# Kernel tuning notes

Hardware: AMD Instinct MI355X
Metric: run time of the kernel (lower is better)

Reference implementation:

```python
import jax, jax.numpy as jnp
import numpy as np

B, H, LQ, LKV, D = 2, 4, 512, 512, 64


def setup_inputs() -> dict:
    key = jax.random.key(0)
    ks = jax.random.split(key, 6)
    queries = jax.random.normal(ks[0], (B, H, LQ, D), dtype=jnp.float32)
    keys = jax.random.normal(ks[1], (B, H, LKV, D), dtype=jnp.float32)
    values = jax.random.normal(ks[2], (B, H, LKV, D), dtype=jnp.float32)
    mask = jax.random.randint(ks[3], (B, LQ, LKV), 0, 2) > 0  # bool [B, Lq, Lkv]
    # linear_concat: weight [D, 2D] (normal std=0.02), bias zeros
    W_concat = jax.random.normal(ks[4], (D, 2 * D), dtype=jnp.float32) * 0.02
    b_concat = jnp.zeros((D,), dtype=jnp.float32)
    # linear_logit: weight [1, D] -> vector [D], bias scalar zero
    w_logit = jax.random.normal(ks[5], (D,), dtype=jnp.float32) * 0.02
    b_logit = jnp.zeros((), dtype=jnp.float32)
    return dict(queries=queries, keys=keys, values=values, mask=mask,
                W_concat=W_concat, b_concat=b_concat,
                w_logit=w_logit, b_logit=b_logit)


def reference(queries, keys, values, mask, W_concat, b_concat, w_logit, b_logit):
    d = queries.shape[-1]
    # cat(q, k) @ W.T == q @ W[:, :d].T + k @ W[:, d:].T  (exact split of the concat-linear)
    qp = jnp.einsum('bhqd,ed->bhqe', queries, W_concat[:, :d])   # [B,H,Lq,D]
    kp = jnp.einsum('bhkd,ed->bhke', keys, W_concat[:, d:])      # [B,H,Lkv,D]
    combined = jnp.tanh(qp[:, :, :, None, :] + kp[:, :, None, :, :] + b_concat)  # [B,H,Lq,Lkv,D]
    logits = jnp.einsum('bhqke,e->bhqk', combined, w_logit) + b_logit            # [B,H,Lq,Lkv]
    # mask handling: invert; rows fully masked get un-masked (avoid all -inf softmax)
    inv = ~mask  # [B,Lq,Lkv]
    inv = jnp.where(jnp.all(inv, axis=-1, keepdims=True), False, inv)
    inv = inv[:, None, :, :]  # broadcast over heads
    logits = jnp.where(inv, -jnp.inf, logits)
    weights = jax.nn.softmax(logits, axis=-1)
    if weights.shape[1] == 1:  # torch .squeeze(dim=1) semantics
        weights = jnp.squeeze(weights, axis=1)
    return weights
```

## Files before the change

kernel.cpp:

```cpp
#include <hip/hip_runtime.h>
#include <hip/hip_bf16.h>


#define NQROWS 4096

typedef float f32x2 __attribute__((ext_vector_type(2)));

__device__ __forceinline__ f32x2 fma2(f32x2 a, f32x2 b, f32x2 c) {
  return __builtin_elementwise_fma(a, b, c);
}
__device__ __forceinline__ f32x2 s2(float x) { return (f32x2){x, x}; }

__global__ __launch_bounds__(256) void proj_kernel(
    const float* __restrict__ Q, const float* __restrict__ K,
    const float* __restrict__ W, const float* __restrict__ bC,
    float* __restrict__ eq, float* __restrict__ ekt)
{
  const int t  = threadIdx.x;
  const int tr = t >> 6;
  const int e  = t & 63;
  const int rbase = blockIdx.x * 8;
  const bool isK = rbase >= NQROWS;
  const int r0 = isK ? rbase - NQROWS : rbase;
  const float* __restrict__ src = isK ? K : Q;
  const int off = isK ? 64 : 0;

  __shared__ float  srow[8][64];
  __shared__ float4 wsh[64][16];
  __shared__ float  trsp[64][9];

  for (int i = t; i < 8 * 64; i += 256)
    srow[i >> 6][i & 63] = src[(r0 + (i >> 6)) * 64 + (i & 63)];
  for (int i = t; i < 64 * 16; i += 256) {
    const int er = i >> 4, d4 = i & 15;
    wsh[er][d4 ^ (er & 7)] =
        reinterpret_cast<const float4*>(W + er * 128 + off)[d4];
  }
  __syncthreads();

  float acc0 = 0.f, acc1 = 0.f;
  const int rA = tr * 2;
  #pragma unroll
  for (int d4 = 0; d4 < 16; ++d4) {
    const float4 w4 = wsh[e][d4 ^ (e & 7)];
    const float4 s0 = *reinterpret_cast<const float4*>(&srow[rA + 0][d4 * 4]);
    const float4 s1 = *reinterpret_cast<const float4*>(&srow[rA + 1][d4 * 4]);
    acc0 = fmaf(s0.x, w4.x, acc0); acc0 = fmaf(s0.y, w4.y, acc0);
    acc0 = fmaf(s0.z, w4.z, acc0); acc0 = fmaf(s0.w, w4.w, acc0);
    acc1 = fmaf(s1.x, w4.x, acc1); acc1 = fmaf(s1.y, w4.y, acc1);
    acc1 = fmaf(s1.z, w4.z, acc1); acc1 = fmaf(s1.w, w4.w, acc1);
  }

  const float C2 = 2.8853900817779268f;
  if (!isK) {
    const float bias = bC[e];
    eq[(r0 + rA + 0) * 64 + e] = __builtin_amdgcn_exp2f((acc0 + bias) * C2);
    eq[(r0 + rA + 1) * 64 + e] = __builtin_amdgcn_exp2f((acc1 + bias) * C2);
  } else {
    trsp[e][rA + 0] = __builtin_amdgcn_exp2f(acc0 * C2);
    trsp[e][rA + 1] = __builtin_amdgcn_exp2f(acc1 * C2);
    __syncthreads();
    const int bh = r0 >> 9;
    const int k0 = r0 & 511;
    float* __restrict__ dst = ekt + bh * 64 * 512 + k0;
    #pragma unroll
    for (int iter = 0; iter < 2; ++iter) {
      const int i  = t + iter * 256;
      const int e2 = i >> 3, kk = i & 7;
      dst[e2 * 512 + kk] = trsp[e2][kk];
    }
  }
}

__global__ __launch_bounds__(256) void attn_kernel(
    const float* __restrict__ eq, const float* __restrict__ ekt,
    const float* __restrict__ wl, const int* __restrict__ mask,
    float* __restrict__ out)
{
  const int t  = threadIdx.x;
  const int c  = t;
  const int wv = t >> 6;
  const int ln = t & 63;
  const int bh = blockIdx.x & 7;
  const int qg = blockIdx.x >> 3;
  const int b  = bh >> 2;
  const int q0 = qg * 4;

  __shared__ float qsh[4][64];
  __shared__ float w2s[64];
  __shared__ float s_sm[4][4], s_sr[4][4];
  __shared__ int   s_any[4][4];

  if (t < 64) w2s[t] = -2.0f * wl[t];
  qsh[t >> 6][t & 63] = eq[(bh * 512 + q0 + (t >> 6)) * 64 + (t & 63)];
  __syncthreads();

  const f32x2* __restrict__ kq =
      reinterpret_cast<const f32x2*>(ekt + bh * 64 * 512) + c;

  f32x2 a0 = {0.f, 0.f}, a1 = {0.f, 0.f}, a2 = {0.f, 0.f}, a3 = {0.f, 0.f};
  const f32x2 one = {1.f, 1.f};

#define QK2(AC, QV)                                                           \
  {                                                                           \
    const f32x2 t0 = fma2(s2(QV.x), Ka, one);                                 \
    const f32x2 t1 = fma2(s2(QV.y), Kb, one);                                 \
    const f32x2 t2 = fma2(s2(QV.z), Kc, one);                                 \
    const f32x2 t3 = fma2(s2(QV.w), Kd, one);                                 \
    const f32x2 t01 = t0 * t1, t23 = t2 * t3;                                 \
    const f32x2 den = t01 * t23;                                              \
    const f32x2 n01 = fma2(s2(w4.x), t1, s2(w4.y) * t0);                      \
    const f32x2 n23 = fma2(s2(w4.z), t3, s2(w4.w) * t2);                      \
    const f32x2 num = fma2(n01, t23, n23 * t01);                              \
    f32x2 r;                                                                  \
    r.x = __builtin_amdgcn_rcpf(den.x);                                       \
    r.y = __builtin_amdgcn_rcpf(den.y);                                       \
    AC = fma2(num, r, AC);                                                    \
  }

  #pragma unroll 4
  for (int eb = 0; eb < 16; ++eb) {
    const f32x2 Ka = kq[(eb * 4 + 0) * 256];
    const f32x2 Kb = kq[(eb * 4 + 1) * 256];
    const f32x2 Kc = kq[(eb * 4 + 2) * 256];
    const f32x2 Kd = kq[(eb * 4 + 3) * 256];
    const float4 qa = *reinterpret_cast<const float4*>(&qsh[0][eb * 4]);
    const float4 qb = *reinterpret_cast<const float4*>(&qsh[1][eb * 4]);
    const float4 qc = *reinterpret_cast<const float4*>(&qsh[2][eb * 4]);
    const float4 qd = *reinterpret_cast<const float4*>(&qsh[3][eb * 4]);
    const float4 w4 = *reinterpret_cast<const float4*>(&w2s[eb * 4]);
    QK2(a0, qa)
    QK2(a1, qb)
    QK2(a2, qc)
    QK2(a3, qd)
  }

  const int* __restrict__ mb = mask + (b * 512 + q0) * 512 + 2 * c;
  const int2 mv0 = *reinterpret_cast<const int2*>(mb);
  const int2 mv1 = *reinterpret_cast<const int2*>(mb + 512);
  const int2 mv2 = *reinterpret_cast<const int2*>(mb + 1024);
  const int2 mv3 = *reinterpret_cast<const int2*>(mb + 1536);

  const float L2E = 1.4426950408889634f;
  f32x2 p0, p1, p2, p3;
  p0.x = __builtin_amdgcn_exp2f(a0.x * L2E);
  p0.y = __builtin_amdgcn_exp2f(a0.y * L2E);
  p1.x = __builtin_amdgcn_exp2f(a1.x * L2E);
  p1.y = __builtin_amdgcn_exp2f(a1.y * L2E);
  p2.x = __builtin_amdgcn_exp2f(a2.x * L2E);
  p2.y = __builtin_amdgcn_exp2f(a2.y * L2E);
  p3.x = __builtin_amdgcn_exp2f(a3.x * L2E);
  p3.y = __builtin_amdgcn_exp2f(a3.y * L2E);

  float sm0 = (mv0.x ? p0.x : 0.f) + (mv0.y ? p0.y : 0.f);
  float sm1 = (mv1.x ? p1.x : 0.f) + (mv1.y ? p1.y : 0.f);
  float sm2 = (mv2.x ? p2.x : 0.f) + (mv2.y ? p2.y : 0.f);
  float sm3 = (mv3.x ? p3.x : 0.f) + (mv3.y ? p3.y : 0.f);
  float sr0 = p0.x + p0.y;
  float sr1 = p1.x + p1.y;
  float sr2 = p2.x + p2.y;
  float sr3 = p3.x + p3.y;
  const int any0 = __any((mv0.x | mv0.y) != 0) ? 1 : 0;
  const int any1 = __any((mv1.x | mv1.y) != 0) ? 1 : 0;
  const int any2 = __any((mv2.x | mv2.y) != 0) ? 1 : 0;
  const int any3 = __any((mv3.x | mv3.y) != 0) ? 1 : 0;

  #pragma unroll
  for (int s = 1; s < 64; s <<= 1) {
    sm0 += __shfl_xor(sm0, s); sm1 += __shfl_xor(sm1, s);
    sm2 += __shfl_xor(sm2, s); sm3 += __shfl_xor(sm3, s);
    sr0 += __shfl_xor(sr0, s); sr1 += __shfl_xor(sr1, s);
    sr2 += __shfl_xor(sr2, s); sr3 += __shfl_xor(sr3, s);
  }
  if (ln == 0) {
    s_sm[wv][0] = sm0; s_sm[wv][1] = sm1; s_sm[wv][2] = sm2; s_sm[wv][3] = sm3;
    s_sr[wv][0] = sr0; s_sr[wv][1] = sr1; s_sr[wv][2] = sr2; s_sr[wv][3] = sr3;
    s_any[wv][0] = any0; s_any[wv][1] = any1;
    s_any[wv][2] = any2; s_any[wv][3] = any3;
  }
  __syncthreads();

#define ROWOUT(P, MV, I)                                                      \
  {                                                                           \
    const bool ra =                                                           \
        (s_any[0][I] | s_any[1][I] | s_any[2][I] | s_any[3][I]) != 0;         \
    const float sm =                                                          \
        (s_sm[0][I] + s_sm[1][I]) + (s_sm[2][I] + s_sm[3][I]);                \
    const float sr =                                                          \
        (s_sr[0][I] + s_sr[1][I]) + (s_sr[2][I] + s_sr[3][I]);                \
    const float inv = 1.0f / (ra ? sm : sr);                                  \
    float2 o2;                                                                \
    o2.x = ((!ra || MV.x) ? P.x : 0.f) * inv;                                 \
    o2.y = ((!ra || MV.y) ? P.y : 0.f) * inv;                                 \
    *reinterpret_cast<float2*>(                                               \
        out + (bh * 512 + q0 + (I)) * 512 + 2 * c) = o2;                      \
  }
  ROWOUT(p0, mv0, 0)
  ROWOUT(p1, mv1, 1)
  ROWOUT(p2, mv2, 2)
  ROWOUT(p3, mv3, 3)
}

extern "C" void kernel_launch(void* const* d_in, const int* in_sizes, int n_in,
                              void* d_out, int out_size, void* d_ws, size_t ws_size,
                              hipStream_t stream) {
  const float* Q  = (const float*)d_in[0];
  const float* K  = (const float*)d_in[1];
  const int*   M  = (const int*)d_in[3];
  const float* W  = (const float*)d_in[4];
  const float* bC = (const float*)d_in[5];
  const float* wl = (const float*)d_in[6];
  float* out = (float*)d_out;
  float* eqbuf  = (float*)d_ws;
  float* ektbuf = eqbuf + NQROWS * 64;

  proj_kernel<<<1024, 256, 0, stream>>>(Q, K, W, bC, eqbuf, ektbuf);
  attn_kernel<<<1024, 256, 0, stream>>>(eqbuf, ektbuf, wl, M, out);
}
```

Baseline: 27.38 us.

## Halve query rows per attention block, read q and w directly, fold scale into exp

The attention kernel now handles 2 query rows per block instead of 4 and launches twice as many blocks. The shared-memory staging of q rows and the scaled logit weights is removed along with its barrier; q and w are read straight from global memory with wave-uniform float4 loads. The -2 factor on w is folded into the exp2 constant instead. This raises parallelism and removes a sync, but each block now reuses each K load for only 2 query rows instead of 4, so total K traffic doubles.

```diff
diff --git a/kernel.cpp b/kernel.cpp
--- a/kernel.cpp
+++ b/kernel.cpp
@@ -82,23 +82,20 @@
   const int wv = t >> 6;
   const int ln = t & 63;
   const int bh = blockIdx.x & 7;
-  const int qg = blockIdx.x >> 3;
+  const int qp = blockIdx.x >> 3;
   const int b  = bh >> 2;
-  const int q0 = qg * 4;
+  const int q0 = qp * 2;
 
-  __shared__ float qsh[4][64];
-  __shared__ float w2s[64];
-  __shared__ float s_sm[4][4], s_sr[4][4];
-  __shared__ int   s_any[4][4];
+  __shared__ float s_sm[4][2], s_sr[4][2];
+  __shared__ int   s_any[4][2];
 
-  if (t < 64) w2s[t] = -2.0f * wl[t];
-  qsh[t >> 6][t & 63] = eq[(bh * 512 + q0 + (t >> 6)) * 64 + (t & 63)];
-  __syncthreads();
+  const float* __restrict__ eqA = eq + (bh * 512 + q0) * 64;
+  const float* __restrict__ eqB = eqA + 64;
 
   const f32x2* __restrict__ kq =
       reinterpret_cast<const f32x2*>(ekt + bh * 64 * 512) + c;
 
-  f32x2 a0 = {0.f, 0.f}, a1 = {0.f, 0.f}, a2 = {0.f, 0.f}, a3 = {0.f, 0.f};
+  f32x2 a0 = {0.f, 0.f}, a1 = {0.f, 0.f};
   const f32x2 one = {1.f, 1.f};
 
 #define QK2(AC, QV)                                                           \
@@ -124,59 +121,40 @@
     const f32x2 Kb = kq[(eb * 4 + 1) * 256];
     const f32x2 Kc = kq[(eb * 4 + 2) * 256];
     const f32x2 Kd = kq[(eb * 4 + 3) * 256];
-    const float4 qa = *reinterpret_cast<const float4*>(&qsh[0][eb * 4]);
-    const float4 qb = *reinterpret_cast<const float4*>(&qsh[1][eb * 4]);
-    const float4 qc = *reinterpret_cast<const float4*>(&qsh[2][eb * 4]);
-    const float4 qd = *reinterpret_cast<const float4*>(&qsh[3][eb * 4]);
-    const float4 w4 = *reinterpret_cast<const float4*>(&w2s[eb * 4]);
+    const float4 qa = *reinterpret_cast<const float4*>(eqA + eb * 4);
+    const float4 qb = *reinterpret_cast<const float4*>(eqB + eb * 4);
+    const float4 w4 = *reinterpret_cast<const float4*>(wl + eb * 4);
     QK2(a0, qa)
     QK2(a1, qb)
-    QK2(a2, qc)
-    QK2(a3, qd)
   }
 
   const int* __restrict__ mb = mask + (b * 512 + q0) * 512 + 2 * c;
   const int2 mv0 = *reinterpret_cast<const int2*>(mb);
   const int2 mv1 = *reinterpret_cast<const int2*>(mb + 512);
-  const int2 mv2 = *reinterpret_cast<const int2*>(mb + 1024);
-  const int2 mv3 = *reinterpret_cast<const int2*>(mb + 1536);
 
-  const float L2E = 1.4426950408889634f;
-  f32x2 p0, p1, p2, p3;
-  p0.x = __builtin_amdgcn_exp2f(a0.x * L2E);
-  p0.y = __builtin_amdgcn_exp2f(a0.y * L2E);
-  p1.x = __builtin_amdgcn_exp2f(a1.x * L2E);
-  p1.y = __builtin_amdgcn_exp2f(a1.y * L2E);
-  p2.x = __builtin_amdgcn_exp2f(a2.x * L2E);
-  p2.y = __builtin_amdgcn_exp2f(a2.y * L2E);
-  p3.x = __builtin_amdgcn_exp2f(a3.x * L2E);
-  p3.y = __builtin_amdgcn_exp2f(a3.y * L2E);
+  const float CM2 = -2.8853900817779268f;
+  f32x2 p0, p1;
+  p0.x = __builtin_amdgcn_exp2f(a0.x * CM2);
+  p0.y = __builtin_amdgcn_exp2f(a0.y * CM2);
+  p1.x = __builtin_amdgcn_exp2f(a1.x * CM2);
+  p1.y = __builtin_amdgcn_exp2f(a1.y * CM2);
 
   float sm0 = (mv0.x ? p0.x : 0.f) + (mv0.y ? p0.y : 0.f);
   float sm1 = (mv1.x ? p1.x : 0.f) + (mv1.y ? p1.y : 0.f);
-  float sm2 = (mv2.x ? p2.x : 0.f) + (mv2.y ? p2.y : 0.f);
-  float sm3 = (mv3.x ? p3.x : 0.f) + (mv3.y ? p3.y : 0.f);
   float sr0 = p0.x + p0.y;
   float sr1 = p1.x + p1.y;
-  float sr2 = p2.x + p2.y;
-  float sr3 = p3.x + p3.y;
   const int any0 = __any((mv0.x | mv0.y) != 0) ? 1 : 0;
   const int any1 = __any((mv1.x | mv1.y) != 0) ? 1 : 0;
-  const int any2 = __any((mv2.x | mv2.y) != 0) ? 1 : 0;
-  const int any3 = __any((mv3.x | mv3.y) != 0) ? 1 : 0;
 
   #pragma unroll
   for (int s = 1; s < 64; s <<= 1) {
     sm0 += __shfl_xor(sm0, s); sm1 += __shfl_xor(sm1, s);
-    sm2 += __shfl_xor(sm2, s); sm3 += __shfl_xor(sm3, s);
     sr0 += __shfl_xor(sr0, s); sr1 += __shfl_xor(sr1, s);
-    sr2 += __shfl_xor(sr2, s); sr3 += __shfl_xor(sr3, s);
   }
   if (ln == 0) {
-    s_sm[wv][0] = sm0; s_sm[wv][1] = sm1; s_sm[wv][2] = sm2; s_sm[wv][3] = sm3;
-    s_sr[wv][0] = sr0; s_sr[wv][1] = sr1; s_sr[wv][2] = sr2; s_sr[wv][3] = sr3;
+    s_sm[wv][0] = sm0; s_sm[wv][1] = sm1;
+    s_sr[wv][0] = sr0; s_sr[wv][1] = sr1;
     s_any[wv][0] = any0; s_any[wv][1] = any1;
-    s_any[wv][2] = any2; s_any[wv][3] = any3;
   }
   __syncthreads();
 
@@ -197,8 +175,6 @@
   }
   ROWOUT(p0, mv0, 0)
   ROWOUT(p1, mv1, 1)
-  ROWOUT(p2, mv2, 2)
-  ROWOUT(p3, mv3, 3)
 }
 
 extern "C" void kernel_launch(void* const* d_in, const int* in_sizes, int n_in,
@@ -215,5 +191,5 @@
   float* ektbuf = eqbuf + NQROWS * 64;
 
   proj_kernel<<<1024, 256, 0, stream>>>(Q, K, W, bC, eqbuf, ektbuf);
-  attn_kernel<<<1024, 256, 0, stream>>>(eqbuf, ektbuf, wl, M, out);
+  attn_kernel<<<2048, 256, 0, stream>>>(eqbuf, ektbuf, wl, M, out);
 }
```

After: 30.18 us. +10.2%, slower.
